# Kernel optimization log

Hardware: AMD Instinct MI355X
Metric: run time of the kernel (lower is better)

Reference implementation:

```python
import jax, jax.numpy as jnp
import numpy as np

B, S, D, H = 2, 2048, 1024, 16
DH = D // H  # per-head dim = 64


def setup_inputs() -> dict:
    key = jax.random.key(0)
    k0, k1, k2, k3, k4, k5 = jax.random.split(key, 6)
    x = jax.random.normal(k0, (B, S, D), dtype=jnp.float32)
    # mask: True where token is valid, False where padded ([B, S, 1] bool)
    mask = jax.random.randint(k1, (B, S, 1), 0, 2).astype(bool)
    scale = 0.02
    # Per-head projection weights stacked over heads: [H, D, DH]
    Wq = jax.random.normal(k2, (H, D, DH), dtype=jnp.float32) * scale
    Wk = jax.random.normal(k3, (H, D, DH), dtype=jnp.float32) * scale
    Wv = jax.random.normal(k4, (H, D, DH), dtype=jnp.float32) * scale
    # Output projection, torch Linear convention [out, in]: y = out @ Wo.T
    Wo = jax.random.normal(k5, (D, D), dtype=jnp.float32) * scale
    return {"x": x, "mask": mask, "Wq": Wq, "Wk": Wk, "Wv": Wv, "Wo": Wo}


def reference(x, mask, Wq, Wk, Wv, Wo):
    # Batched per-head projections (equivalent to the per-head Linear loop)
    q = jnp.einsum('bsd,hde->bhse', x, Wq)  # [B,H,S,DH]
    k = jnp.einsum('bsd,hde->bhse', x, Wk)
    v = jnp.einsum('bsd,hde->bhse', x, Wv)
    scale = 1.0 / np.sqrt(DH).astype(np.float32)
    scores = jnp.einsum('bhqe,bhke->bhqk', q, k) * scale  # [B,H,S,S]
    key_mask = mask[:, None, None, :, 0]   # [B,1,1,S]
    qry_mask = mask[:, None, :, :]          # [B,1,S,1]
    # masked keys get -1e10 added (same as original: +(~key_mask)*-1e10)
    scores = scores + (~key_mask) * jnp.float32(-1e10)
    attn = jax.nn.softmax(scores, axis=-1)
    attn = attn * qry_mask                  # zero rows for padded queries
    ctx = jnp.einsum('bhqk,bhke->bhqe', attn, v)  # [B,H,S,DH]
    # concat heads along last dim (head h -> contiguous slice, matches torch.cat)
    out = ctx.transpose(0, 2, 1, 3).reshape(B, S, D)
    return out @ Wo.T
```

## Files before the change

### kernel.cpp

```cpp
#include <hip/hip_runtime.h>
#include <hip/hip_bf16.h>

typedef __attribute__((ext_vector_type(8))) short sh8;
typedef __attribute__((ext_vector_type(4))) float f32x4;

#define LDC 136
#define QSCALE 0.18033688f
#define KMBF16 0xF14Au

#define EXP2F(x) __builtin_amdgcn_exp2f(x)

__device__ __forceinline__ void glds16(const unsigned short* g, unsigned short* l){
  __builtin_amdgcn_global_load_lds(
      (const __attribute__((address_space(1))) unsigned int*)g,
      (__attribute__((address_space(3))) unsigned int*)l, 16, 0, 0);
}

__device__ __forceinline__ unsigned short f2bf(float f){
  union { float f; unsigned u; } c; c.f = f;
  unsigned u = c.u;
  u += 0x7fffu + ((u >> 16) & 1u);
  return (unsigned short)(u >> 16);
}

__device__ __forceinline__ unsigned long long pack4bf(float a, float b, float c, float d){
  __hip_bfloat162 lo = __float22bfloat162_rn(make_float2(a, b));
  __hip_bfloat162 hi = __float22bfloat162_rn(make_float2(c, d));
  union { unsigned u[2]; unsigned long long ull; } pk;
  pk.u[0] = *(unsigned*)&lo; pk.u[1] = *(unsigned*)&hi;
  return pk.ull;
}

__global__ __launch_bounds__(256) void cvt_bf16_2(const float* __restrict__ s0,
                                                  unsigned short* __restrict__ d0, int n0,
                                                  const float* __restrict__ s1,
                                                  unsigned short* __restrict__ d1, int n1){
  int i = blockIdx.x*256 + threadIdx.x;
  const float* s; unsigned short* d;
  if (i < n0){ s = s0; d = d0; }
  else if (i < n0 + n1){ s = s1; d = d1; i -= n0; }
  else return;
  float4 v = ((const float4*)s)[i];
  ushort4 o;
  o.x = f2bf(v.x); o.y = f2bf(v.y); o.z = f2bf(v.z); o.w = f2bf(v.w);
  ((ushort4*)d)[i] = o;
}

__global__ __launch_bounds__(256) void transpose_w(const float* __restrict__ Wq,
                                                   const float* __restrict__ Wk,
                                                   const float* __restrict__ Wv,
                                                   unsigned short* __restrict__ wt){
  __shared__ float tile[64][65];
  int idx = blockIdx.x;
  int jm = idx >> 8;
  int rest = idx & 255;
  int h = rest >> 4, dt = rest & 15;
  const float* src = (jm==0 ? Wq : (jm==1 ? Wk : Wv)) + (size_t)h*65536;
  int t = threadIdx.x;
  {
    int r = t >> 2, c0 = (t & 3)*16;
    for (int i=0;i<4;++i){
      float4 v = *(const float4*)&src[(size_t)(dt*64 + r)*64 + c0 + i*4];
      tile[r][c0+i*4+0]=v.x; tile[r][c0+i*4+1]=v.y; tile[r][c0+i*4+2]=v.z; tile[r][c0+i*4+3]=v.w;
    }
  }
  __syncthreads();
  {
    int e = t >> 2, r0 = (t & 3)*16;
    int j = jm*1024 + h*64 + e;
    __align__(16) unsigned short buf[16];
    for (int i=0;i<16;++i) buf[i] = f2bf(tile[r0+i][e]);
    *(uint4*)&wt[(size_t)j*1024 + dt*64 + r0    ] = *(uint4*)&buf[0];
    *(uint4*)&wt[(size_t)j*1024 + dt*64 + r0 + 8] = *(uint4*)&buf[8];
  }
}

__global__ __launch_bounds__(64) void mask_scan(const int* __restrict__ mask,
                                                int* __restrict__ pidx){
  int b = blockIdx.x, lane = threadIdx.x;
  int m[32];
  #pragma unroll
  for (int c = 0; c < 32; ++c) m[c] = mask[b*2048 + c*64 + lane];
  int base = 0;
  #pragma unroll
  for (int c = 0; c < 32; ++c){
    unsigned long long bal = __ballot(m[c] != 0);
    int pos = base + (int)__popcll(bal & ((1ULL << lane) - 1ULL));
    pidx[b*2048 + c*64 + lane] = m[c] ? pos : -1;
    base += (int)__popcll(bal);
  }
}

template<int BM>
__global__ __launch_bounds__(256) void gemm_bt(const unsigned short* __restrict__ A,
                                               const unsigned short* __restrict__ Bt,
                                               unsigned short* __restrict__ Cq,
                                               unsigned short* __restrict__ Ck,
                                               unsigned short* __restrict__ Cv,
                                               float* __restrict__ Cf,
                                               const int* __restrict__ pidx,
                                               int M, int N, int K, int mode){
  constexpr int MI = BM/32;
  constexpr int ABUF = BM*64;
  constexpr int DBUFN = 2*ABUF + 2*8192;
  constexpr int SMEMN = (DBUFN > 17664) ? DBUFN : 17664;
  __shared__ __align__(16) unsigned short smem[SMEMN];
  const int t = threadIdx.x;
  const int w = t >> 6, lane = t & 63, l15 = lane & 15, quad = lane >> 4;

  int lin = blockIdx.y * gridDim.x + blockIdx.x;
  int gn = gridDim.x;
  int per = 8 * gn;
  int gid = lin / per, rem = lin % per;
  int j = rem / gn, nc = rem % gn;
  const int m0 = (gid*8 + j) * BM;
  const int n0 = nc * 128;

  const int wm = (w >> 1)*(BM/2), wn = (w & 1)*64;
  const int lr8 = lane >> 3;
  const int gc8 = (lane & 7) ^ lr8;
  const int h7 = l15 & 7;
  f32x4 acc[MI][4] = {};

  auto stage = [&](int k0, int bb){
    unsigned short* as = smem + bb*ABUF;
    unsigned short* bs = smem + 2*ABUF + bb*8192;
    for (int p = 0; p < BM/32; ++p){
      int rbase = p*32 + w*8;
      glds16(&A [(size_t)(m0 + rbase + lr8)*K + k0 + gc8*8], &as[rbase*64]);
    }
    for (int p = 0; p < 4; ++p){
      int rbase = p*32 + w*8;
      glds16(&Bt[(size_t)(n0 + rbase + lr8)*K + k0 + gc8*8], &bs[rbase*64]);
    }
  };

  const int NS = K >> 6;
  stage(0, 0);
  for (int ks = 0; ks < NS; ++ks){
    const int bb = ks & 1;
    __syncthreads();
    if (ks + 1 < NS) stage((ks+1)*64, bb ^ 1);
    const unsigned short* as = smem + bb*ABUF;
    const unsigned short* bs = smem + 2*ABUF + bb*8192;
    for (int kk = 0; kk < 2; ++kk){
      const int cs = (((kk<<2) + quad) ^ h7) * 8;
      sh8 aF[MI], bF[4];
      for (int i = 0; i < MI; ++i)
        aF[i] = *(const sh8*)&as[(wm + i*16 + l15)*64 + cs];
      for (int i = 0; i < 4; ++i)
        bF[i] = *(const sh8*)&bs[(wn + i*16 + l15)*64 + cs];
      for (int mi = 0; mi < MI; ++mi)
        for (int ni = 0; ni < 4; ++ni)
          acc[mi][ni] = __builtin_amdgcn_mfma_f32_16x16x32_bf16(aF[mi], bF[ni], acc[mi][ni], 0, 0, 0);
    }
  }

  if (mode == 2){
    for (int mi = 0; mi < MI; ++mi){
      int rowb = m0 + wm + mi*16 + quad*4;
      for (int ni = 0; ni < 4; ++ni){
        int col = n0 + wn + ni*16 + l15;
        for (int r = 0; r < 4; ++r)
          Cf[(size_t)(rowb + r)*N + col] = acc[mi][ni][r];
      }
    }
    return;
  }

  if constexpr (BM == 128){
    __syncthreads();
    unsigned short* Ct = smem;
    int* pS = (int*)(smem + 17408);
    const bool isv = (n0 >= 2048);
    const float cscale = (n0 < 1024) ? QSCALE : 1.0f;
    const int b = m0 >> 11, sbase = m0 & 2047;
    for (int mi = 0; mi < 4; ++mi){
      for (int ni = 0; ni < 4; ++ni){
        for (int r = 0; r < 4; ++r){
          int lr = wm + mi*16 + quad*4 + r;
          int lc = wn + ni*16 + l15;
          unsigned short bv = f2bf(acc[mi][ni][r] * cscale);
          if (isv) Ct[lc*LDC + lr] = bv;
          else     Ct[lr*LDC + lc] = bv;
        }
      }
    }
    if (t < 128) pS[t] = pidx[b*2048 + sbase + t];
    __syncthreads();

    const int hbase = (n0 & 1023) >> 6;
    if (!isv){
      const bool isq = (n0 < 1024);
      unsigned short* dst = isq ? Cq : Ck;
      for (int i = 0; i < 8; ++i){
        int s  = i*16 + (t >> 4);
        int hh = (t >> 3) & 1;
        int c  = t & 7;
        uint4 val = *(const uint4*)&Ct[s*LDC + hh*64 + c*8];
        int h = hbase + hh;
        int row;
        if (isq) row = sbase + s;
        else { int p = pS[s]; if (p < 0) continue; row = p; }
        *(uint4*)&dst[((size_t)(b*16 + h)*2048 + row)*64 + c*8] = val;
      }
    } else {
      for (int i = 0; i < 8; ++i){
        int ecol = i*16 + (t >> 4);
        int s0   = (t & 15)*8;
        int hh = ecol >> 6, e = ecol & 63;
        int h = hbase + hh;
        unsigned short* dr = &Cv[((size_t)(b*16 + h)*64 + e)*2048];
        union { uint4 v; unsigned short us[8]; } val;
        val.v = *(const uint4*)&Ct[ecol*LDC + s0];
        #pragma unroll
        for (int jj = 0; jj < 8; ++jj){
          int p = pS[s0 + jj];
          if (p >= 0) dr[p] = val.us[jj];
        }
      }
    }
  }
}

__global__ __launch_bounds__(512) void flash_attn(const unsigned short* __restrict__ q,
                                                  const unsigned short* __restrict__ k,
                                                  const unsigned short* __restrict__ vt,
                                                  const int* __restrict__ mask,
                                                  unsigned short* __restrict__ ctx){
  __shared__ __align__(16) unsigned short Ks[2][4096];
  __shared__ __align__(16) unsigned short Vs[2][4096];
  __shared__ __align__(16) unsigned short Ps[8][1024];
  __shared__ __align__(16) unsigned short kmb[2048];
  __shared__ int s_nv;

  const int idx = blockIdx.x;
  const int xcd = idx & 7, sub = idx >> 3;
  const int bh = xcd*4 + (sub & 3);
  const int qt = sub >> 2;
  const int b = bh >> 4, h = bh & 15;
  const int t = threadIdx.x;
  const int w = t >> 6, lane = t & 63, l15 = lane & 15, quad = lane >> 4;
  const size_t base = (size_t)bh * 2048 * 64;

  const unsigned short* qp0 = q + base + (size_t)(qt*128 + w*16 + l15)*64;
  sh8 qf[2];
  qf[0] = *(const sh8*)(qp0 +      quad*8);
  qf[1] = *(const sh8*)(qp0 + 32 + quad*8);

  if (t == 0) s_nv = 0;
  int4 mv = ((const int4*)(mask + b*2048))[t];
  __syncthreads();
  {
    int c = (mv.x != 0) + (mv.y != 0) + (mv.z != 0) + (mv.w != 0);
    c += __shfl_down(c, 32); c += __shfl_down(c, 16); c += __shfl_down(c, 8);
    c += __shfl_down(c, 4);  c += __shfl_down(c, 2);  c += __shfl_down(c, 1);
    if (lane == 0) atomicAdd(&s_nv, c);
  }
  __syncthreads();
  const int nv = s_nv;
  const int ntiles = (nv + 63) >> 6;

  {
    __align__(8) unsigned short tmp[4];
    #pragma unroll
    for (int i = 0; i < 4; ++i) tmp[i] = (t*4 + i < nv) ? 0 : (unsigned short)KMBF16;
    *(unsigned long long*)&kmb[t*4] = *(unsigned long long*)tmp;
  }

  const int lr8 = lane >> 3;
  const int gc8 = (lane & 7) ^ lr8;
  const int h7 = l15 & 7;
  const int cs0 = ((quad    ) ^ h7) * 8;
  const int cs1 = ((quad + 4) ^ h7) * 8;
  const int pw_off = (quad & 1)*4;
  const int pr0 = ((0*4 + quad) ^ h7) * 8;
  const int pr1 = ((1*4 + quad) ^ h7) * 8;

  auto stageKV = [&](int kt, int bb){
    int r0 = w*8;
    glds16(&k [base + (size_t)(kt*64 + r0 + lr8)*64 + gc8*8], &Ks[bb][r0*64]);
    glds16(&vt[base + (size_t)(r0 + lr8)*2048 + kt*64 + gc8*8], &Vs[bb][r0*64]);
  };

  float la[4] = {};
  f32x4 O[4] = {};

  if (ntiles > 0) stageKV(0, 0);
  for (int kt = 0; kt < ntiles; ++kt){
    const int bb = kt & 1;
    __syncthreads();
    if (kt + 1 < ntiles) stageKV(kt + 1, bb ^ 1);

    for (int mt = 0; mt < 4; ++mt){
      sh8 a0 = *(const sh8*)&Ks[bb][(mt*16 + l15)*64 + cs0];
      sh8 a1 = *(const sh8*)&Ks[bb][(mt*16 + l15)*64 + cs1];
      unsigned long long kq = *(const unsigned long long*)&kmb[kt*64 + mt*16 + quad*4];
      unsigned d0 = (unsigned)kq, d1 = (unsigned)(kq >> 32);
      f32x4 a;
      a[0] = __uint_as_float(d0 << 16);
      a[1] = __uint_as_float(d0 & 0xFFFF0000u);
      a[2] = __uint_as_float(d1 << 16);
      a[3] = __uint_as_float(d1 & 0xFFFF0000u);
      const int pwc = (((mt*2 + (quad>>1)) ^ h7) * 8) + pw_off;
      a = __builtin_amdgcn_mfma_f32_16x16x32_bf16(a0, qf[0], a, 0, 0, 0);
      a = __builtin_amdgcn_mfma_f32_16x16x32_bf16(a1, qf[1], a, 0, 0, 0);
      float e0 = EXP2F(a[0]); la[0] += e0;
      float e1 = EXP2F(a[1]); la[1] += e1;
      float e2 = EXP2F(a[2]); la[2] += e2;
      float e3 = EXP2F(a[3]); la[3] += e3;
      *(unsigned long long*)&Ps[w][l15*64 + pwc] = pack4bf(e0, e1, e2, e3);
    }

    sh8 pf0 = *(const sh8*)&Ps[w][l15*64 + pr0];
    sh8 pf1 = *(const sh8*)&Ps[w][l15*64 + pr1];
    for (int et = 0; et < 4; ++et){
      sh8 vf0 = *(const sh8*)&Vs[bb][(et*16 + l15)*64 + cs0];
      O[et] = __builtin_amdgcn_mfma_f32_16x16x32_bf16(vf0, pf0, O[et], 0, 0, 0);
    }
    for (int et = 0; et < 4; ++et){
      sh8 vf1 = *(const sh8*)&Vs[bb][(et*16 + l15)*64 + cs1];
      O[et] = __builtin_amdgcn_mfma_f32_16x16x32_bf16(vf1, pf1, O[et], 0, 0, 0);
    }
  }

  {
    float l_i = (la[0] + la[1]) + (la[2] + la[3]);
    l_i += __shfl_xor(l_i, 16);
    l_i += __shfl_xor(l_i, 32);
    int srow = qt*128 + w*16 + l15;
    bool qm = (mask[b*2048 + srow] != 0);
    float inv = (qm && l_i > 0.f) ? 1.f/l_i : 0.f;
    unsigned short* crow = ctx + (((size_t)b*2048 + srow)*16 + h)*64;
    for (int et = 0; et < 4; ++et)
      *(unsigned long long*)&crow[et*16 + quad*4] =
        pack4bf(O[et][0]*inv, O[et][1]*inv, O[et][2]*inv, O[et][3]*inv);
  }
}

extern "C" void kernel_launch(void* const* d_in, const int* in_sizes, int n_in,
                              void* d_out, int out_size, void* d_ws, size_t ws_size,
                              hipStream_t stream){
  const float* x  = (const float*)d_in[0];
  const int* mask = (const int*)  d_in[1];
  const float* Wq = (const float*)d_in[2];
  const float* Wk = (const float*)d_in[3];
  const float* Wv = (const float*)d_in[4];
  const float* Wo = (const float*)d_in[5];
  float* out = (float*)d_out;

  char* ws = (char*)d_ws;
  unsigned short* x_bf  = (unsigned short*)(ws);
  unsigned short* wt    = (unsigned short*)(ws + 8388608);
  unsigned short* wo_bf = (unsigned short*)(ws + 14680064);
  unsigned short* qb    = (unsigned short*)(ws + 16777216);
  unsigned short* kb    = (unsigned short*)(ws + 25165824);
  unsigned short* vtb   = (unsigned short*)(ws + 33554432);
  unsigned short* ctx   = (unsigned short*)(ws + 41943040);
  int*            pidx  = (int*)(ws + 41943040);

  hipMemsetAsync(ws + 25165824, 0, 16777216, stream);
  mask_scan<<<2, 64, 0, stream>>>(mask, pidx);
  cvt_bf16_2<<<5120, 256, 0, stream>>>(x, x_bf, 1048576, Wo, wo_bf, 262144);
  transpose_w<<<768, 256, 0, stream>>>(Wq, Wk, Wv, wt);
  gemm_bt<128><<<dim3(24, 32), 256, 0, stream>>>(x_bf, wt, qb, kb, vtb, nullptr, pidx, 4096, 3072, 1024, 0);
  flash_attn<<<512, 512, 0, stream>>>(qb, kb, vtb, mask, ctx);
  gemm_bt<64><<<dim3(8, 64), 256, 0, stream>>>(ctx, wo_bf, nullptr, nullptr, nullptr, out, pidx, 4096, 1024, 1024, 2);
}
```

Baseline: 177.4 us.

## Triple-buffer GEMM K-loop with 32-wide K tiles and explicit vmcnt waits

The GEMM main loop moves from double-buffered 64-wide K stages to triple-buffered 32-wide K stages. Loads run two stages ahead, and a partial s_waitcnt vmcnt followed by a raw s_barrier replaces the full __syncthreads. The LDS swizzle is reworked for 32-element rows. The aim is to overlap more of the global-to-LDS latency with MFMA work, at the cost of twice as many barrier iterations and hand-tuned wait counts that depend on the exact number of loads issued per stage.

```diff
diff --git a/kernel.cpp b/kernel.cpp
--- a/kernel.cpp
+++ b/kernel.cpp
@@ -101,9 +101,11 @@
                                                const int* __restrict__ pidx,
                                                int M, int N, int K, int mode){
   constexpr int MI = BM/32;
-  constexpr int ABUF = BM*64;
-  constexpr int DBUFN = 2*ABUF + 2*8192;
-  constexpr int SMEMN = (DBUFN > 17664) ? DBUFN : 17664;
+  constexpr int ABUF = BM*32;
+  constexpr int BBUF = 128*32;
+  constexpr int BUFN = ABUF + BBUF;
+  constexpr int TOTN = 3*BUFN;
+  constexpr int SMEMN = (TOTN > 17664) ? TOTN : 17664;
   __shared__ __align__(16) unsigned short smem[SMEMN];
   const int t = threadIdx.x;
   const int w = t >> 6, lane = t & 63, l15 = lane & 15, quad = lane >> 4;
@@ -117,43 +119,52 @@
   const int n0 = nc * 128;
 
   const int wm = (w >> 1)*(BM/2), wn = (w & 1)*64;
-  const int lr8 = lane >> 3;
-  const int gc8 = (lane & 7) ^ lr8;
-  const int h7 = l15 & 7;
+  const int lr16 = lane >> 2;
+  const int gcq  = (lane & 3) ^ ((lane >> 2) & 3) ^ ((lane >> 4) & 3);
+  const int cs   = ((quad ^ (l15 & 3) ^ ((l15 >> 2) & 3)) << 3);
   f32x4 acc[MI][4] = {};
 
   auto stage = [&](int k0, int bb){
-    unsigned short* as = smem + bb*ABUF;
-    unsigned short* bs = smem + 2*ABUF + bb*8192;
-    for (int p = 0; p < BM/32; ++p){
-      int rbase = p*32 + w*8;
-      glds16(&A [(size_t)(m0 + rbase + lr8)*K + k0 + gc8*8], &as[rbase*64]);
-    }
-    for (int p = 0; p < 4; ++p){
-      int rbase = p*32 + w*8;
-      glds16(&Bt[(size_t)(n0 + rbase + lr8)*K + k0 + gc8*8], &bs[rbase*64]);
+    unsigned short* as = smem + bb*BUFN;
+    unsigned short* bs = as + ABUF;
+    for (int p = 0; p < BM/64; ++p){
+      int r0 = w*(BM/4) + p*16;
+      glds16(&A [(size_t)(m0 + r0 + lr16)*K + k0 + gcq*8], &as[r0*32]);
+    }
+    for (int p = 0; p < 2; ++p){
+      int r0 = w*32 + p*16;
+      glds16(&Bt[(size_t)(n0 + r0 + lr16)*K + k0 + gcq*8], &bs[r0*32]);
     }
   };
 
-  const int NS = K >> 6;
+  const int NS = K >> 5;
   stage(0, 0);
+  stage(32, 1);
+  int cb = 0, sb = 2;
   for (int ks = 0; ks < NS; ++ks){
-    const int bb = ks & 1;
-    __syncthreads();
-    if (ks + 1 < NS) stage((ks+1)*64, bb ^ 1);
-    const unsigned short* as = smem + bb*ABUF;
-    const unsigned short* bs = smem + 2*ABUF + bb*8192;
-    for (int kk = 0; kk < 2; ++kk){
-      const int cs = (((kk<<2) + quad) ^ h7) * 8;
-      sh8 aF[MI], bF[4];
-      for (int i = 0; i < MI; ++i)
-        aF[i] = *(const sh8*)&as[(wm + i*16 + l15)*64 + cs];
-      for (int i = 0; i < 4; ++i)
-        bF[i] = *(const sh8*)&bs[(wn + i*16 + l15)*64 + cs];
-      for (int mi = 0; mi < MI; ++mi)
-        for (int ni = 0; ni < 4; ++ni)
-          acc[mi][ni] = __builtin_amdgcn_mfma_f32_16x16x32_bf16(aF[mi], bF[ni], acc[mi][ni], 0, 0, 0);
-    }
+    if (ks == NS - 1){
+      asm volatile("s_waitcnt vmcnt(0)" ::: "memory");
+    } else {
+      if constexpr (BM == 128) asm volatile("s_waitcnt vmcnt(4)" ::: "memory");
+      else                     asm volatile("s_waitcnt vmcnt(3)" ::: "memory");
+    }
+    __builtin_amdgcn_s_barrier();
+    __builtin_amdgcn_sched_barrier(0);
+    if (ks + 2 < NS) stage((ks+2)*32, sb);
+
+    const unsigned short* as = smem + cb*BUFN;
+    const unsigned short* bs = as + ABUF;
+    sh8 aF[MI], bF[4];
+    for (int i = 0; i < MI; ++i)
+      aF[i] = *(const sh8*)&as[(wm + i*16 + l15)*32 + cs];
+    for (int i = 0; i < 4; ++i)
+      bF[i] = *(const sh8*)&bs[(wn + i*16 + l15)*32 + cs];
+    for (int mi = 0; mi < MI; ++mi)
+      for (int ni = 0; ni < 4; ++ni)
+        acc[mi][ni] = __builtin_amdgcn_mfma_f32_16x16x32_bf16(aF[mi], bF[ni], acc[mi][ni], 0, 0, 0);
+
+    cb = (cb == 2) ? 0 : cb + 1;
+    sb = (sb == 2) ? 0 : sb + 1;
   }
 
   if (mode == 2){
```

Result: no change. 179.8 us (+1.4%).

## Prefetch two K-stages ahead in GEMM with explicit vmcnt waits

Applied to the files above, without the earlier changes.

Restructures the GEMM main loop so the next two K tiles are prefetched. Each iteration first loads all LDS fragments into registers, then releases the buffer with a barrier so the next global-to-LDS load can start before the MFMAs run. Explicit s_waitcnt vmcnt counts replace the plain __syncthreads, keeping more loads in flight. In exchange it holds more fragment registers and relies on hand-counted vmcnt values being correct for each BM.

```diff
diff --git a/kernel.cpp b/kernel.cpp
--- a/kernel.cpp
+++ b/kernel.cpp
@@ -102,8 +102,10 @@
                                                int M, int N, int K, int mode){
   constexpr int MI = BM/32;
   constexpr int ABUF = BM*64;
-  constexpr int DBUFN = 2*ABUF + 2*8192;
-  constexpr int SMEMN = (DBUFN > 17664) ? DBUFN : 17664;
+  constexpr int BBUF = 128*64;
+  constexpr int BUFN = ABUF + BBUF;
+  constexpr int TOTN = 2*BUFN;
+  constexpr int SMEMN = (TOTN > 17664) ? TOTN : 17664;
   __shared__ __align__(16) unsigned short smem[SMEMN];
   const int t = threadIdx.x;
   const int w = t >> 6, lane = t & 63, l15 = lane & 15, quad = lane >> 4;
@@ -123,8 +125,8 @@
   f32x4 acc[MI][4] = {};
 
   auto stage = [&](int k0, int bb){
-    unsigned short* as = smem + bb*ABUF;
-    unsigned short* bs = smem + 2*ABUF + bb*8192;
+    unsigned short* as = smem + bb*BUFN;
+    unsigned short* bs = as + ABUF;
     for (int p = 0; p < BM/32; ++p){
       int rbase = p*32 + w*8;
       glds16(&A [(size_t)(m0 + rbase + lr8)*K + k0 + gc8*8], &as[rbase*64]);
@@ -137,23 +139,40 @@
 
   const int NS = K >> 6;
   stage(0, 0);
+  stage(64, 1);
   for (int ks = 0; ks < NS; ++ks){
-    const int bb = ks & 1;
-    __syncthreads();
-    if (ks + 1 < NS) stage((ks+1)*64, bb ^ 1);
-    const unsigned short* as = smem + bb*ABUF;
-    const unsigned short* bs = smem + 2*ABUF + bb*8192;
+    const int cb = ks & 1;
+    if (ks == NS - 1){
+      asm volatile("s_waitcnt vmcnt(0)" ::: "memory");
+    } else {
+      if constexpr (BM == 128) asm volatile("s_waitcnt vmcnt(8)" ::: "memory");
+      else                     asm volatile("s_waitcnt vmcnt(6)" ::: "memory");
+    }
+    __builtin_amdgcn_s_barrier();
+    __builtin_amdgcn_sched_barrier(0);
+
+    const unsigned short* as = smem + cb*BUFN;
+    const unsigned short* bs = as + ABUF;
+    sh8 aF[2][MI], bF[2][4];
+    #pragma unroll
     for (int kk = 0; kk < 2; ++kk){
       const int cs = (((kk<<2) + quad) ^ h7) * 8;
-      sh8 aF[MI], bF[4];
       for (int i = 0; i < MI; ++i)
-        aF[i] = *(const sh8*)&as[(wm + i*16 + l15)*64 + cs];
+        aF[kk][i] = *(const sh8*)&as[(wm + i*16 + l15)*64 + cs];
       for (int i = 0; i < 4; ++i)
-        bF[i] = *(const sh8*)&bs[(wn + i*16 + l15)*64 + cs];
+        bF[kk][i] = *(const sh8*)&bs[(wn + i*16 + l15)*64 + cs];
+    }
+    asm volatile("s_waitcnt lgkmcnt(0)" ::: "memory");
+    __builtin_amdgcn_sched_barrier(0);
+    __builtin_amdgcn_s_barrier();
+    __builtin_amdgcn_sched_barrier(0);
+    if (ks + 2 < NS) stage((ks+2)*64, cb);
+
+    #pragma unroll
+    for (int kk = 0; kk < 2; ++kk)
       for (int mi = 0; mi < MI; ++mi)
         for (int ni = 0; ni < 4; ++ni)
-          acc[mi][ni] = __builtin_amdgcn_mfma_f32_16x16x32_bf16(aF[mi], bF[ni], acc[mi][ni], 0, 0, 0);
-    }
+          acc[mi][ni] = __builtin_amdgcn_mfma_f32_16x16x32_bf16(aF[kk][mi], bF[kk][ni], acc[mi][ni], 0, 0, 0);
   }
 
   if (mode == 2){
```

After: 181.2 us. 2.2% more time.
